# Optimization experiments

Hardware: AMD Instinct MI355X
Metric: run time of the kernel (lower is better)

Reference implementation:

```python
import jax, jax.numpy as jnp
import numpy as np

# Hyperparameters matching init_kwargs
DIM = 1024
HEADS = 16
MEM_HIDDEN = 512
FF_DIM = 4096
CHUNK = 128
NPERSIST = 16
ALPHA = 0.02
THETA = 0.1
ETA = 0.9
B, T = 2, 1024


def _mem_read(x, p):
    """DeepMemory forward: 2-layer MLP dim->hidden->dim with SiLU between."""
    W1, b1, W2, b2 = p
    h = jax.nn.silu(x @ W1.T + b1)
    return h @ W2.T + b2


def setup_inputs() -> dict:
    key = jax.random.key(0)
    ks = jax.random.split(key, 16)
    s = 0.02  # weight init scale
    return {
        "x": jax.random.normal(ks[0], (B, T, DIM), jnp.float32),
        "Wqkv": jax.random.normal(ks[1], (3 * DIM, DIM), jnp.float32) * s,
        "mW1": jax.random.normal(ks[2], (MEM_HIDDEN, DIM), jnp.float32) * s,
        "mb1": jnp.zeros((MEM_HIDDEN,), jnp.float32),
        "mW2": jax.random.normal(ks[3], (DIM, MEM_HIDDEN), jnp.float32) * s,
        "mb2": jnp.zeros((DIM,), jnp.float32),
        "P": jax.random.normal(ks[4], (1, NPERSIST, DIM), jnp.float32),
        "Wqkv_attn": jax.random.normal(ks[5], (3 * DIM, DIM), jnp.float32) * s,
        "Wo": jax.random.normal(ks[6], (DIM, DIM), jnp.float32) * s,
        "ffW1": jax.random.normal(ks[7], (FF_DIM, DIM), jnp.float32) * s,
        "ffb1": jnp.zeros((FF_DIM,), jnp.float32),
        "ffW2": jax.random.normal(ks[8], (DIM, FF_DIM), jnp.float32) * s,
        "ffb2": jnp.zeros((DIM,), jnp.float32),
    }


def reference(x, Wqkv, mW1, mb1, mW2, mb2, P, Wqkv_attn, Wo, ffW1, ffb1, ffW2, ffb2):
    Bb, Tt, D = x.shape
    nC = Tt // CHUNK

    # shared qkv projection (bias-free Linear)
    qkv = x @ Wqkv.T                       # [B,T,3D]
    K = qkv[..., D:2 * D]
    V = qkv[..., 2 * D:]

    # chunked test-time memory writes: k,v are detached in the torch code
    Kc = jax.lax.stop_gradient(K).reshape(Bb, nC, CHUNK, D).transpose(1, 0, 2, 3)  # [nC,B,C,D]
    Vc = jax.lax.stop_gradient(V).reshape(Bb, nC, CHUNK, D).transpose(1, 0, 2, 3)

    params0 = tuple(jax.lax.stop_gradient(p) for p in (mW1, mb1, mW2, mb2))
    mom0 = tuple(jnp.zeros_like(p) for p in params0)

    def loss_fn(p, k, v):
        return jnp.mean((_mem_read(k, p) - v) ** 2)

    def step(carry, kv):
        p, m = carry
        k, v = kv
        g = jax.grad(loss_fn)(p, k, v)
        # momentum: s = eta*s - theta*g ; weight: w = (1-alpha)*w + s
        m = tuple(ETA * mi - THETA * gi for mi, gi in zip(m, g))
        p = tuple((1.0 - ALPHA) * pi + mi for pi, mi in zip(p, m))
        return (p, m), None

    (pf, _), _ = jax.lax.scan(step, (params0, mom0), (Kc, Vc))
    pf = jax.lax.stop_gradient(pf)  # fast weights are buffers (non-differentiable)

    # memory readout tokens for the whole segment
    Q = qkv[..., :D]
    mem_tok = _mem_read(Q, pf)             # [B,T,D]

    # concatenate persistent + memory + input tokens
    tokens = jnp.concatenate([jnp.broadcast_to(P, (Bb, NPERSIST, D)), mem_tok, x], axis=1)
    N = tokens.shape[1]                    # NPERSIST + 2T
    dh = D // HEADS

    # causal multi-head attention over the concatenated sequence
    aqkv = tokens @ Wqkv_attn.T            # [B,N,3D]
    q, k, v = jnp.split(aqkv, 3, axis=-1)
    to_heads = lambda t: t.reshape(Bb, N, HEADS, dh).transpose(0, 2, 1, 3)
    q, k, v = to_heads(q), to_heads(k), to_heads(v)
    scores = jnp.einsum('bhnd,bhmd->bhnm', q, k) / jnp.sqrt(jnp.float32(dh))
    causal = jnp.tril(jnp.ones((N, N), bool))
    scores = jnp.where(causal, scores, jnp.float32(-1e9))
    attn = jax.nn.softmax(scores, axis=-1)
    o = jnp.einsum('bhnm,bhmd->bhnd', attn, v).transpose(0, 2, 1, 3).reshape(Bb, N, D)
    y = o @ Wo.T

    # feed-forward (no residual in source)
    y = jax.nn.gelu(y @ ffW1.T + ffb1) @ ffW2.T + ffb2

    # drop persistent + memory tokens, gate by a fresh memory read
    out = y[:, NPERSIST + Tt:, :]          # [B,T,D]
    newQ = (out @ Wqkv.T)[..., :D]
    return out * _mem_read(newQ, pf)
```

## Files before the change

### kernel.cpp

```cpp
#include <hip/hip_runtime.h>
#include <math.h>

#define BATCH 2
#define TSEQ 1024
#define DIMD 1024
#define NPERS 16
#define NCH 8
#define NTOK 2064
#define ETA_C 0.9f
#define THETA_C 0.1f
#define ALPHA_C 0.02f

typedef __attribute__((ext_vector_type(4))) float f32x4;
typedef __attribute__((ext_vector_type(8))) short s16x8;
typedef unsigned short u16;

__device__ __forceinline__ u16 f2bf(float f) {
    unsigned int u = __float_as_uint(f);
    return (u16)((u + 0x7fffu + ((u >> 16) & 1u)) >> 16);
}
__device__ __forceinline__ float bf2f(u16 h) { return __uint_as_float(((unsigned)h) << 16); }
__device__ __forceinline__ void split2(float v, u16& h, u16& l) {
    h = f2bf(v); l = f2bf(v - bf2f(h));
}

static const size_t oRA = 0;
static const size_t oRB = 50724864;
static const size_t oRC = 67633152;
static const size_t oRD = 80216064;
static const size_t oRE = 96993280;
static const size_t oRF = 109576192;
static const size_t oRG = 113770496;
static const size_t oRH = 117970944;

static const size_t PW1 = 0, PB1 = 524288, PW2 = 524800, PB2 = 1049088, PSZ = 1050112;

__device__ __forceinline__ void gload_lds16(const u16* g, u16* l) {
    __builtin_amdgcn_global_load_lds(
        (const __attribute__((address_space(1))) unsigned int*)g,
        (__attribute__((address_space(3))) unsigned int*)l, 16, 0, 0);
}

__device__ __forceinline__ void xcd_swz2(int cmaj, int& bx, int& by) {
    int gx = gridDim.x, gy = gridDim.y, nwg = gx * gy;
    int lid = cmaj ? (blockIdx.x * gy + blockIdx.y) : (blockIdx.y * gx + blockIdx.x);
    int t = lid;
    if ((nwg & 7) == 0) {
        int q = nwg >> 3;
        t = (lid & 7) * q + (lid >> 3);
    }
    if (cmaj) { by = t % gy; bx = t / gy; }
    else      { bx = t % gx; by = t / gx; }
}
__device__ __forceinline__ void xcd_swizzle(int& bx, int& by) { xcd_swz2(0, bx, by); }

__device__ __forceinline__ void stage_tile(const u16* sp, u16* buf, int rbase,
                                           int M, int clampM, int K, int k0,
                                           int lane) {
    const int lr = lane >> 2, lc = lane & 3;
    #pragma unroll
    for (int i = 0; i < 8; ++i) {
        int r = i * 16 + lr;
        int gr = rbase + r;
        if (clampM && gr >= M) gr = M - 1;
        int g = lc ^ ((r >> 1) & 3);
        gload_lds16(sp + (size_t)gr * K + k0 + g * 8, buf + i * 512);
    }
}

__device__ __forceinline__ void stage_tile64(const u16* sp, u16* buf, int rbase,
                                             int K, int k0, int lane) {
    const int lr = lane >> 3, lc = lane & 7;
    #pragma unroll
    for (int i = 0; i < 16; ++i) {
        int r = i * 8 + lr;
        int gr = rbase + r;
        int g = lc ^ (r & 7);
        gload_lds16(sp + (size_t)gr * K + k0 + g * 8, buf + i * 512);
    }
}

template<int NPROD>
__device__ __forceinline__ void mm_loop32(u16* lds,
                const u16* sp, int rbase, int M, int clampM, int K,
                int kbeg, int kend, int wid, int lane, int wm, int wn,
                f32x4 acc[4][4]) {
    constexpr int TILES = (NPROD == 3) ? 4 : 3;
    constexpr int BUF = TILES * 4096;
    constexpr int WOFF = (NPROD == 3) ? 2 : 1;
    const int frow = lane & 15, kblk = lane >> 4;
    const int nt = (kend - kbeg) >> 5;
    const int doStage = (NPROD == 3) || (wid != 1);
    const int stile = (NPROD == 3) ? wid : ((wid == 0) ? 0 : wid - 1);
    if (doStage) stage_tile(sp, lds + stile * 4096, rbase, M, clampM, K, kbeg, lane);
    for (int t = 0; t < nt; ++t) {
        __syncthreads();
        if (t + 1 < nt && doStage)
            stage_tile(sp, lds + ((t + 1) & 1) * BUF + stile * 4096, rbase, M, clampM, K,
                       kbeg + ((t + 1) << 5), lane);
        const u16* cb = lds + (t & 1) * BUF;
        s16x8 bh[4], bl[4];
        #pragma unroll
        for (int ni = 0; ni < 4; ++ni) {
            int br = wn * 64 + ni * 16 + frow;
            int pc = kblk ^ ((br >> 1) & 3);
            bh[ni] = *(const s16x8*)&cb[WOFF * 4096 + br * 32 + pc * 8];
            bl[ni] = *(const s16x8*)&cb[(WOFF + 1) * 4096 + br * 32 + pc * 8];
        }
        #pragma unroll
        for (int mi = 0; mi < 4; ++mi) {
            int ar = wm * 64 + mi * 16 + frow;
            int pc = kblk ^ ((ar >> 1) & 3);
            s16x8 ah = *(const s16x8*)&cb[0 * 4096 + ar * 32 + pc * 8];
            s16x8 al;
            if (NPROD == 3) al = *(const s16x8*)&cb[1 * 4096 + ar * 32 + pc * 8];
            #pragma unroll
            for (int ni = 0; ni < 4; ++ni) {
                acc[mi][ni] = __builtin_amdgcn_mfma_f32_16x16x32_bf16(ah, bh[ni], acc[mi][ni], 0, 0, 0);
                acc[mi][ni] = __builtin_amdgcn_mfma_f32_16x16x32_bf16(ah, bl[ni], acc[mi][ni], 0, 0, 0);
                if (NPROD == 3)
                    acc[mi][ni] = __builtin_amdgcn_mfma_f32_16x16x32_bf16(al, bh[ni], acc[mi][ni], 0, 0, 0);
            }
        }
    }
}

template<int ACTF, int WF32, int WSPLIT, int PARTIAL, int NPROD>
__global__ __launch_bounds__(256)
void gemm_mfma_k(const u16* __restrict__ Ah, const u16* __restrict__ Al,
                 const u16* __restrict__ Wh, const u16* __restrict__ Wl,
                 float* __restrict__ C, u16* __restrict__ Chi, u16* __restrict__ Clo,
                 int M, int N, int K, const float* __restrict__ bias, int cmaj)
{
    constexpr int TILES = (NPROD == 3) ? 4 : 3;
    __shared__ u16 lds[2 * TILES * 4096];
    const int tid = threadIdx.x;
    const int lane = tid & 63, wid = tid >> 6;
    const int wm = wid >> 1, wn = wid & 1;
    int bx, by; xcd_swz2(cmaj, bx, by);
    const int row0 = by * 128, col0 = bx * 128;
    const u16* sp = (wid == 0) ? Ah : (wid == 1) ? Al : (wid == 2) ? Wh : Wl;
    const int rbase = (wid < 2) ? row0 : col0;
    const int clampM = (wid < 2) ? 1 : 0;
    f32x4 acc[4][4] = {};
    int kbeg = 0, kend = K;
    if (PARTIAL) {
        int Kseg = K / gridDim.z;
        kbeg = blockIdx.z * Kseg;
        kend = kbeg + Kseg;
    }
    mm_loop32<NPROD>(&lds[0], sp, rbase, M, clampM, K, kbeg, kend, wid, lane, wm, wn, acc);

    const int erow = (lane >> 4) * 4, ecol = lane & 15;
    #pragma unroll
    for (int mi = 0; mi < 4; ++mi) {
        #pragma unroll
        for (int ni = 0; ni < 4; ++ni) {
            int c = col0 + wn * 64 + ni * 16 + ecol;
            float bv = (!PARTIAL && bias) ? bias[c] : 0.f;
            #pragma unroll
            for (int reg = 0; reg < 4; ++reg) {
                int r = row0 + wm * 64 + mi * 16 + erow + reg;
                if (r >= M) continue;
                float v = acc[mi][ni][reg] + bv;
                if (PARTIAL) {
                    C[((size_t)blockIdx.z * M + r) * N + c] = v;
                    continue;
                }
                if (ACTF == 1) v = v / (1.f + __expf(-v));
                else if (ACTF == 2) {
                    float u = 0.7978845608028654f * (v + 0.044715f * v * v * v);
                    v = 0.5f * v * (1.f + tanhf(u));
                }
                size_t o = (size_t)r * N + c;
                if (WF32) C[o] = v;
                if (WSPLIT) { u16 h, l; split2(v, h, l); Chi[o] = h; Clo[o] = l; }
            }
        }
    }
}

__global__ __launch_bounds__(256)
void gemm_qkv_k(const u16* __restrict__ Ah, const u16* __restrict__ Al,
                const u16* __restrict__ Wh, const u16* __restrict__ Wl,
                u16* __restrict__ Qh, u16* __restrict__ Ql,
                u16* __restrict__ kch, u16* __restrict__ kcl,
                u16* __restrict__ kcTh, u16* __restrict__ kcTl,
                float* __restrict__ Vb, int M, int N, int K)
{
    __shared__ u16 lds[2 * 3 * 4096];
    const int tid = threadIdx.x;
    const int lane = tid & 63, wid = tid >> 6;
    const int wm = wid >> 1, wn = wid & 1;
    int bx, by; xcd_swz2(1, bx, by);
    const int row0 = by * 128, col0 = bx * 128;
    const u16* sp = (wid == 0) ? Ah : (wid == 1) ? Al : (wid == 2) ? Wh : Wl;
    const int rbase = (wid < 2) ? row0 : col0;
    f32x4 acc[4][4] = {};
    mm_loop32<2>(&lds[0], sp, rbase, M, 0, K, 0, K, wid, lane, wm, wn, acc);

    const int erow = (lane >> 4) * 4, ecol = lane & 15;
    #pragma unroll
    for (int mi = 0; mi < 4; ++mi) {
        #pragma unroll
        for (int ni = 0; ni < 4; ++ni) {
            int c = col0 + wn * 64 + ni * 16 + ecol;
            #pragma unroll
            for (int reg = 0; reg < 4; ++reg) {
                int r = row0 + wm * 64 + mi * 16 + erow + reg;
                float v = acc[mi][ni][reg];
                int b = r >> 10, t = r & 1023;
                if (c < 1024) {
                    size_t o = (size_t)r * 1024 + c;
                    Qh[o] = f2bf(v);
                } else if (c < 2048) {
                    int d = c - 1024;
                    int ch = t >> 7, rr = t & 127;
                    size_t o = ((size_t)((ch * 2 + b) * 128 + rr)) * 1024 + d;
                    u16 h, l; split2(v, h, l);
                    kch[o] = h;
                    size_t ot = (size_t)ch * 262144 + (size_t)d * 256 + b * 128 + rr;
                    kcTh[ot] = h; kcTl[ot] = l;
                } else {
                    int d = c - 2048;
                    int ch = t >> 7, rr = t & 127;
                    Vb[((size_t)((ch * 2 + b) * 128 + rr)) * 1024 + d] = v;
                }
            }
        }
    }
}

__global__ __launch_bounds__(256)
void gemm_aqkv_k(const u16* __restrict__ Ah, const u16* __restrict__ Al,
                 const u16* __restrict__ Wh, const u16* __restrict__ Wl,
                 u16* __restrict__ fQh, u16* __restrict__ fQl,
                 u16* __restrict__ fKh, u16* __restrict__ fKl,
                 u16* __restrict__ fVt, int M, int N, int K)
{
    __shared__ u16 lds[2 * 3 * 4096];
    const int tid = threadIdx.x;
    const int lane = tid & 63, wid = tid >> 6;
    const int wm = wid >> 1, wn = wid & 1;
    int bx, by; xcd_swz2(1, bx, by);
    if (bx < 8 && ((by <= 7) || (by >= 17 && by <= 23))) return;
    const int row0 = by * 128, col0 = bx * 128;
    const u16* sp = (wid == 0) ? Ah : (wid == 1) ? Al : (wid == 2) ? Wh : Wl;
    const int rbase = (wid < 2) ? row0 : col0;
    const int clampM = (wid < 2) ? 1 : 0;
    f32x4 acc[4][4] = {};
    mm_loop32<2>(&lds[0], sp, rbase, M, clampM, K, 0, K, wid, lane, wm, wn, acc);

    const int erow = (lane >> 4) * 4, ecol = lane & 15;
    #pragma unroll
    for (int mi = 0; mi < 4; ++mi) {
        #pragma unroll
        for (int ni = 0; ni < 4; ++ni) {
            int c = col0 + wn * 64 + ni * 16 + ecol;
            #pragma unroll
            for (int reg = 0; reg < 4; ++reg) {
                int r = row0 + wm * 64 + mi * 16 + erow + reg;
                if (r >= M) continue;
                float v = acc[mi][ni][reg];
                int b = (r >= 2064) ? 1 : 0;
                int n = r - b * 2064;
                if (c < 1024) {
                    if (n >= NPERS + TSEQ) {
                        int h = c >> 6, d = c & 63;
                        int row = n - (NPERS + TSEQ);
                        size_t o = (((size_t)(b * 16 + h)) * 1024 + row) * 64 + d;
                        u16 hh, ll; split2(0.125f * v, hh, ll);
                        fQh[o] = hh; fQl[o] = ll;
                    }
                } else if (c < 2048) {
                    int cc = c - 1024;
                    int h = cc >> 6, d = cc & 63;
                    size_t o = (((size_t)(b * 16 + h)) * NTOK + n) * 64 + d;
                    u16 hh, ll; split2(v, hh, ll);
                    fKh[o] = hh; fKl[o] = ll;
                } else {
                    int cc = c - 2048;
                    int h = cc >> 6, d = cc & 63;
                    fVt[(((size_t)(b * 16 + h)) * 64 + d) * NTOK + n] = f2bf(v);
                }
            }
        }
    }
}

template<int ACTF, int WF32, int WSPLIT>
__global__ __launch_bounds__(256)
void reduce_k(const float* __restrict__ Cp, int S,
              float* __restrict__ C, u16* __restrict__ Chi, u16* __restrict__ Clo,
              const float* __restrict__ bias, int M, int N)
{
    int i = blockIdx.x * 256 + threadIdx.x;
    int n4 = (int)((size_t)M * N / 4);
    if (i >= n4) return;
    size_t off = (size_t)i * 4;
    float4 v = *(const float4*)&Cp[off];
    for (int z = 1; z < S; ++z) {
        float4 u = *(const float4*)&Cp[(size_t)z * M * N + off];
        v.x += u.x; v.y += u.y; v.z += u.z; v.w += u.w;
    }
    int c = (int)(off % N);
    float vv[4] = {v.x, v.y, v.z, v.w};
    #pragma unroll
    for (int j = 0; j < 4; ++j) {
        float w = vv[j];
        if (bias) w += bias[c + j];
        if (ACTF == 1) w = w / (1.f + __expf(-w));
        else if (ACTF == 2) {
            float u = 0.7978845608028654f * (w + 0.044715f * w * w * w);
            w = 0.5f * w * (1.f + tanhf(u));
        }
        if (WF32) C[off + j] = w;
        if (WSPLIT) { u16 h, l; split2(w, h, l); Chi[off + j] = h; Clo[off + j] = l; }
    }
}

__global__ __launch_bounds__(256)
void reduce_tok_k(const float* __restrict__ Cp, const float* __restrict__ bias,
                  u16* __restrict__ th, u16* __restrict__ tl)
{
    int i = blockIdx.x * 256 + threadIdx.x;
    if (i >= 524288) return;
    size_t off = (size_t)i * 4;
    float4 v = *(const float4*)&Cp[off];
    float4 u = *(const float4*)&Cp[2097152 + off];
    v.x += u.x; v.y += u.y; v.z += u.z; v.w += u.w;
    int r = (int)(off >> 10), c = (int)(off & 1023);
    int b = r >> 10, t = r & 1023;
    size_t orow = (((size_t)(b * NTOK + NPERS + t)) << 10) + c;
    float vv[4] = {v.x + bias[c], v.y + bias[c + 1], v.z + bias[c + 2], v.w + bias[c + 3]};
    u16 h0,l0,h1,l1,h2,l2,h3,l3;
    split2(vv[0],h0,l0); split2(vv[1],h1,l1); split2(vv[2],h2,l2); split2(vv[3],h3,l3);
    ushort4 hv = {h0,h1,h2,h3}, lv = {l0,l1,l2,l3};
    *(ushort4*)&th[orow] = hv;
    *(ushort4*)&tl[orow] = lv;
}

static void gemm_mfma(hipStream_t s, int act, int wf32, int wsplit,
                      const u16* Ah, const u16* Al, const u16* Wh, const u16* Wl,
                      float* C, u16* Ch, u16* Cl, int M, int N, int K,
                      const float* bias, int nprod = 3, int cmaj = 0)
{
    dim3 g(N / 128, (M + 127) / 128), b(256);
    if (act == 0 && wf32 == 1 && wsplit == 0)
        gemm_mfma_k<0,1,0,0,3><<<g,b,0,s>>>(Ah,Al,Wh,Wl,C,Ch,Cl,M,N,K,bias,cmaj);
    else if (act == 0 && wf32 == 1 && wsplit == 1)
        gemm_mfma_k<0,1,1,0,3><<<g,b,0,s>>>(Ah,Al,Wh,Wl,C,Ch,Cl,M,N,K,bias,cmaj);
    else if (act == 0 && wf32 == 0 && wsplit == 1)
        gemm_mfma_k<0,0,1,0,3><<<g,b,0,s>>>(Ah,Al,Wh,Wl,C,Ch,Cl,M,N,K,bias,cmaj);
    else if (act == 1)
        gemm_mfma_k<1,0,1,0,3><<<g,b,0,s>>>(Ah,Al,Wh,Wl,C,Ch,Cl,M,N,K,bias,cmaj);
    else if (nprod == 2)
        gemm_mfma_k<2,0,1,0,2><<<g,b,0,s>>>(Ah,Al,Wh,Wl,C,Ch,Cl,M,N,K,bias,cmaj);
    else
        gemm_mfma_k<2,0,1,0,3><<<g,b,0,s>>>(Ah,Al,Wh,Wl,C,Ch,Cl,M,N,K,bias,cmaj);
}

static void gemm_mfma_sk(hipStream_t s, int act, int wf32, int wsplit,
                         const u16* Ah, const u16* Al, const u16* Wh, const u16* Wl,
                         float* C, u16* Ch, u16* Cl, int M, int N, int K,
                         const float* bias, int S, float* part, int nprod = 3,
                         int cmaj = 0)
{
    if (S <= 1) { gemm_mfma(s, act, wf32, wsplit, Ah, Al, Wh, Wl, C, Ch, Cl, M, N, K, bias, nprod, cmaj); return; }
    dim3 g(N / 128, (M + 127) / 128, S), b(256);
    if (nprod == 2)
        gemm_mfma_k<0,0,0,1,2><<<g,b,0,s>>>(Ah,Al,Wh,Wl,part,nullptr,nullptr,M,N,K,nullptr,cmaj);
    else
        gemm_mfma_k<0,0,0,1,3><<<g,b,0,s>>>(Ah,Al,Wh,Wl,part,nullptr,nullptr,M,N,K,nullptr,cmaj);
    int n4 = (int)((size_t)M * N / 4);
    dim3 rg((n4 + 255) / 256), rb(256);
    if (act == 0 && wf32 == 1 && wsplit == 0)
        reduce_k<0,1,0><<<rg,rb,0,s>>>(part, S, C, Ch, Cl, bias, M, N);
    else if (act == 0 && wf32 == 1 && wsplit == 1)
        reduce_k<0,1,1><<<rg,rb,0,s>>>(part, S, C, Ch, Cl, bias, M, N);
    else if (act == 0 && wf32 == 0 && wsplit == 1)
        reduce_k<0,0,1><<<rg,rb,0,s>>>(part, S, C, Ch, Cl, bias, M, N);
    else if (act == 1)
        reduce_k<1,0,1><<<rg,rb,0,s>>>(part, S, C, Ch, Cl, bias, M, N);
    else
        reduce_k<2,0,1><<<rg,rb,0,s>>>(part, S, C, Ch, Cl, bias, M, N);
}

template<int MODE, int NPROD>
__device__ __forceinline__ void scan_body(u16* lds, int bx, int by,
                 const u16* __restrict__ Ah, const u16* __restrict__ Al,
                 const u16* __restrict__ Wh, const u16* __restrict__ Wl,
                 float* __restrict__ C, u16* __restrict__ Chi, u16* __restrict__ Clo,
                 u16* __restrict__ ChiT, u16* __restrict__ CloT,
                 const float* __restrict__ Zf, const float* __restrict__ add,
                 const float* __restrict__ bias, float* __restrict__ CP,
                 int M, int N, int K, float alpha)
{
    constexpr int TILES = (NPROD == 3) ? 4 : 3;
    constexpr int BUF = TILES * 8192;
    constexpr int WOFF = (NPROD == 3) ? 2 : 1;
    const int tid = threadIdx.x;
    const int lane = tid & 63, wid = tid >> 6;
    const int wm = wid >> 1, wn = wid & 1;
    const int row0 = by * 128, col0 = bx * 128;

    const u16* sp = (wid == 0) ? Ah : (wid == 1) ? Al : (wid == 2) ? Wh : Wl;
    const int rbase = (wid < 2) ? row0 : col0;
    const int doStage = (NPROD == 3) || (wid != 1);
    const int stile = (NPROD == 3) ? wid : ((wid == 0) ? 0 : wid - 1);

    f32x4 acc[4][4] = {};
    const int frow = lane & 15, kblk = lane >> 4;
    const int nt = K >> 6;

    if (doStage) stage_tile64(sp, lds + stile * 8192, rbase, K, 0, lane);

    for (int t = 0; t < nt; ++t) {
        __syncthreads();
        if (t + 1 < nt && doStage)
            stage_tile64(sp, lds + ((t + 1) & 1) * BUF + stile * 8192, rbase, K,
                         (t + 1) << 6, lane);
        const u16* cb = lds + (t & 1) * BUF;

        #pragma unroll
        for (int s = 0; s < 2; ++s) {
            s16x8 bh[4], bl[4];
            #pragma unroll
            for (int ni = 0; ni < 4; ++ni) {
                int br = wn * 64 + ni * 16 + frow;
                int pc = (s * 4 + kblk) ^ (br & 7);
                bh[ni] = *(const s16x8*)&cb[WOFF * 8192 + br * 64 + pc * 8];
                bl[ni] = *(const s16x8*)&cb[(WOFF + 1) * 8192 + br * 64 + pc * 8];
            }
            #pragma unroll
            for (int mi = 0; mi < 4; ++mi) {
                int ar = wm * 64 + mi * 16 + frow;
                int pc = (s * 4 + kblk) ^ (ar & 7);
                s16x8 ah = *(const s16x8*)&cb[0 * 8192 + ar * 64 + pc * 8];
                s16x8 al;
                if (NPROD == 3) al = *(const s16x8*)&cb[1 * 8192 + ar * 64 + pc * 8];
                #pragma unroll
                for (int ni = 0; ni < 4; ++ni) {
                    acc[mi][ni] = __builtin_amdgcn_mfma_f32_16x16x32_bf16(ah, bh[ni], acc[mi][ni], 0, 0, 0);
                    acc[mi][ni] = __builtin_amdgcn_mfma_f32_16x16x32_bf16(ah, bl[ni], acc[mi][ni], 0, 0, 0);
                    if (NPROD == 3)
                        acc[mi][ni] = __builtin_amdgcn_mfma_f32_16x16x32_bf16(al, bh[ni], acc[mi][ni], 0, 0, 0);
                }
            }
        }
    }

    const int erow = (lane >> 4) * 4, ecol = lane & 15;
    float csum[4] = {0.f, 0.f, 0.f, 0.f};
    #pragma unroll
    for (int mi = 0; mi < 4; ++mi) {
        #pragma unroll
        for (int ni = 0; ni < 4; ++ni) {
            int c = col0 + wn * 64 + ni * 16 + ecol;
            #pragma unroll
            for (int reg = 0; reg < 4; ++reg) {
                int r = row0 + wm * 64 + mi * 16 + erow + reg;
                float v = acc[mi][ni][reg];
                size_t o = (size_t)r * N + c;
                if (MODE == 1) {
                    v += bias[c];
                    C[o] = v;
                    float hv = v / (1.f + __expf(-v));
                    u16 h, l; split2(hv, h, l);
                    Chi[o] = h; Clo[o] = l;
                    size_t ot = (size_t)c * M + r;
                    ChiT[ot] = h; CloT[ot] = l;
                } else if (MODE == 2) {
                    v += bias[c] - add[o];
                    u16 h, l; split2(v, h, l);
                    Chi[o] = h; Clo[o] = l;
                    size_t ot = (size_t)c * M + r;
                    ChiT[ot] = h; CloT[ot] = l;
                    csum[ni] += v;
                } else if (MODE == 3) {
                    C[o] = alpha * v;
                } else {
                    v *= alpha;
                    float z = Zf[o];
                    float sg = 1.f / (1.f + __expf(-z));
                    v *= sg * (1.f + z * (1.f - sg));
                    u16 h, l; split2(v, h, l);
                    size_t ot = (size_t)c * M + r;
                    ChiT[ot] = h; CloT[ot] = l;
                    csum[ni] += v;
                }
            }
        }
    }
    if (MODE == 2 || MODE == 4) {
        #pragma unroll
        for (int ni = 0; ni < 4; ++ni) {
            float s = csum[ni];
            s += __shfl_xor(s, 16);
            s += __shfl_xor(s, 32);
            if ((lane >> 4) == 0) {
                int c = col0 + wn * 64 + ni * 16 + ecol;
                float w = (MODE == 2) ? alpha * s : s;
                CP[(size_t)(by * 2 + wm) * N + c] = w;
            }
        }
    }
}

template<int MODE>
__global__ __launch_bounds__(256)
void gemm_scan_k(const u16* __restrict__ Ah, const u16* __restrict__ Al,
                 const u16* __restrict__ Wh, const u16* __restrict__ Wl,
                 float* __restrict__ C, u16* __restrict__ Chi, u16* __restrict__ Clo,
                 u16* __restrict__ ChiT, u16* __restrict__ CloT,
                 const float* __restrict__ Zf, const float* __restrict__ add,
                 const float* __restrict__ bias, float* __restrict__ CP,
                 int M, int N, int K, float alpha)
{
    __shared__ u16 lds[2 * 3 * 8192];
    int bx, by; xcd_swizzle(bx, by);
    scan_body<MODE, 2>(&lds[0], bx, by, Ah, Al, Wh, Wl, C, Chi, Clo, ChiT, CloT,
                       Zf, add, bias, CP, M, N, K, alpha);
}

__global__ __launch_bounds__(256)
void gemm_scan_pair_k(const u16* __restrict__ rTh, const u16* __restrict__ rTl,
                      const u16* __restrict__ hTh, const u16* __restrict__ hTl,
                      float* __restrict__ gW2,
                      const u16* __restrict__ rh_, const u16* __restrict__ rl_,
                      const u16* __restrict__ w2th, const u16* __restrict__ w2tl,
                      u16* __restrict__ dhTh, u16* __restrict__ dhTl,
                      const float* __restrict__ z1, float* __restrict__ cp1, float cs)
{
    __shared__ u16 lds[2 * 3 * 8192];
    if (blockIdx.y < 8) {
        scan_body<3, 2>(&lds[0], blockIdx.x, blockIdx.y, rTh, rTl, hTh, hTl,
                        gW2, nullptr, nullptr, nullptr, nullptr, nullptr, nullptr,
                        nullptr, nullptr, 1024, 512, 256, cs);
    } else {
        scan_body<4, 2>(&lds[0], blockIdx.x, blockIdx.y - 8, rh_, rl_, w2th, w2tl,
                        nullptr, nullptr, nullptr, dhTh, dhTl, z1, nullptr,
                        nullptr, cp1, 256, 512, 1024, cs);
    }
}

__global__ void cvt_split_k(const float* __restrict__ in, u16* __restrict__ hi,
                            u16* __restrict__ lo, int n4) {
    int i = blockIdx.x * 256 + threadIdx.x;
    if (i >= n4) return;
    float4 v = *(const float4*)&in[(size_t)i * 4];
    u16 h0,l0,h1,l1,h2,l2,h3,l3;
    split2(v.x,h0,l0); split2(v.y,h1,l1); split2(v.z,h2,l2); split2(v.w,h3,l3);
    ushort4 hv = {h0,h1,h2,h3}, lv = {l0,l1,l2,l3};
    *(ushort4*)&hi[(size_t)i * 4] = hv;
    *(ushort4*)&lo[(size_t)i * 4] = lv;
}
__global__ void transpose_split_k(const float* __restrict__ in, u16* __restrict__ outh,
                                  u16* __restrict__ outl, int R, int C) {
    __shared__ float t[32][33];
    const int c0 = blockIdx.x * 32, r0 = blockIdx.y * 32;
    const size_t zoff = (size_t)blockIdx.z * R * C;
    const int tx = threadIdx.x & 31, ty = threadIdx.x >> 5;
    #pragma unroll
    for (int p = 0; p < 4; ++p) {
        int r = ty + p * 8;
        t[r][tx] = in[zoff + (size_t)(r0 + r) * C + c0 + tx];
    }
    __syncthreads();
    #pragma unroll
    for (int p = 0; p < 4; ++p) {
        int cc = ty + p * 8;
        float v = t[tx][cc];
        u16 h, l; split2(v, h, l);
        size_t o = zoff + (size_t)(c0 + cc) * R + r0 + tx;
        outh[o] = h; outl[o] = l;
    }
}
__global__ void update3_k(float* __restrict__ p, float* __restrict__ mo,
                          const float* __restrict__ g,
                          const float* __restrict__ cp1, const float* __restrict__ cp2,
                          u16* __restrict__ w1h, u16* __restrict__ w1l,
                          u16* __restrict__ w2h, u16* __restrict__ w2l,
                          u16* __restrict__ w2th, u16* __restrict__ w2tl, int n) {
    int i = blockIdx.x * 256 + threadIdx.x;
    if (i >= n) return;
    float gi;
    if (i < 524288) gi = g[i];
    else if (i < 524800) {
        int j = i - 524288;
        gi = cp1[j] + cp1[512 + j] + cp1[1024 + j] + cp1[1536 + j];
    } else if (i < 1049088) gi = g[i];
    else {
        int j = i - 1049088;
        gi = cp2[j] + cp2[1024 + j] + cp2[2048 + j] + cp2[3072 + j];
    }
    float m = ETA_C * mo[i] - THETA_C * gi;
    mo[i] = m;
    float pv = (1.f - ALPHA_C) * p[i] + m;
    p[i] = pv;
    if (i < 524288) {
        u16 h, l; split2(pv, h, l); w1h[i] = h; w1l[i] = l;
    } else if (i >= 524800 && i < 1049088) {
        int j = i - 524800;
        u16 h, l; split2(pv, h, l);
        w2h[j] = h; w2l[j] = l;
        int tj = (j & 511) * 1024 + (j >> 9);
        w2th[tj] = h; w2tl[tj] = l;
    }
}
__global__ void tokens_px_k(const float* __restrict__ P, const float* __restrict__ x,
                            u16* __restrict__ th, u16* __restrict__ tl) {
    size_t idx = (size_t)blockIdx.x * 256 + threadIdx.x;
    if (idx >= (size_t)2 * 1040 * 1024) return;
    int d = (int)(idx & 1023);
    int rl = (int)((idx >> 10) % 1040);
    int b = (int)(idx / ((size_t)1040 * 1024));
    float v; int n;
    if (rl < NPERS) { v = P[(size_t)rl * 1024 + d]; n = rl; }
    else { int t = rl - NPERS; v = x[((size_t)b * TSEQ + t) * 1024 + d]; n = NPERS + TSEQ + t; }
    size_t o = (((size_t)(b * NTOK + n)) << 10) + d;
    u16 h, l; split2(v, h, l); th[o] = h; tl[o] = l;
}
__global__ void mul_k(const float* __restrict__ a, const float* __restrict__ b,
                      float* __restrict__ o, int n) {
    int i = blockIdx.x * 256 + threadIdx.x;
    if (i < n) o[i] = a[i] * b[i];
}

__global__ __launch_bounds__(256)
void flash_part_k(const u16* __restrict__ Qsh, const u16* __restrict__ Qsl,
                  const u16* __restrict__ Ksh, const u16* __restrict__ Ksl,
                  const u16* __restrict__ Vts, float* __restrict__ Of,
                  float* __restrict__ Lf)
{
    __shared__ u16 lds[16384];
    u16* KH = lds;            u16* KL = lds + 4096;
    u16* VT = lds + 8192;
    u16* PH = lds + 12288;

    int lid = blockIdx.x + (blockIdx.y << 4) + (blockIdx.z << 8);
    int t1024 = ((lid & 7) << 7) | (lid >> 3);
    const int qt = t1024 & 15, h = (t1024 >> 4) & 15;
    const int zb = t1024 >> 8;
    const int b = zb >> 1, z = zb & 1;

    const int tid = threadIdx.x;
    const int lane = tid & 63, wid = tid >> 6;
    const int fr = lane & 15, kq = lane >> 4;
    const int bh = b * 16 + h;
    const int q0c = qt * 64;
    const int q0a = NPERS + TSEQ + q0c;
    const int ntile = ((q0a + 63) >> 6) + 1;
    const int half = ntile >> 1;
    const int jt0 = z ? half : 0;
    const int jt1 = z ? ntile : half;
    const int l8 = lane & 7, lr8 = lane >> 3;

    auto stageKV = [&](int jt) {
        const int j0 = jt * 64;
        #pragma unroll
        for (int jj = 0; jj < 6; ++jj) {
            int j = wid * 6 + jj;
            int buf = j >> 3, i8 = j & 7;
            if (buf < 2) {
                int row = i8 * 8 + lr8;
                int grow = j0 + row; if (grow > NTOK - 1) grow = NTOK - 1;
                int c = l8 ^ (row & 7);
                const u16* src = (buf == 0 ? Ksh : Ksl) +
                                 (((size_t)bh * NTOK + grow) << 6) + c * 8;
                gload_lds16(src, (buf == 0 ? KH : KL) + i8 * 512);
            } else {
                int d = i8 * 8 + lr8;
                int c = l8 ^ (d & 7);
                int col = j0 + c * 8; if (col > NTOK - 8) col = NTOK - 8;
                const u16* src = Vts + ((size_t)bh * 64 + d) * NTOK + col;
                gload_lds16(src, VT + i8 * 512);
            }
        }
    };

    s16x8 qh[2], ql[2];
    {
        const size_t qrow = ((size_t)bh * 1024 + q0c + wid * 16 + fr) << 6;
        #pragma unroll
        for (int kb = 0; kb < 2; ++kb) {
            qh[kb] = *(const s16x8*)&Qsh[qrow + (size_t)(kb * 4 + kq) * 8];
            ql[kb] = *(const s16x8*)&Qsl[qrow + (size_t)(kb * 4 + kq) * 8];
        }
    }

    s16x8 ones;
    #pragma unroll
    for (int i = 0; i < 8; ++i) ones[i] = (short)0x3F80;

    f32x4 Oa[4] = {};
    f32x4 lacc = {};

    for (int jt = jt0; jt < jt1; ++jt) {
        const int j0 = jt * 64;
        stageKV(jt);
        __syncthreads();

        f32x4 sacc[4] = {};
        __builtin_amdgcn_s_setprio(1);
        #pragma unroll
        for (int nt = 0; nt < 4; ++nt) {
            #pragma unroll
            for (int kb = 0; kb < 2; ++kb) {
                int br = nt * 16 + fr;
                int sl = (kb * 4 + kq) ^ (fr & 7);
                s16x8 kh = *(const s16x8*)&KH[br * 64 + sl * 8];
                s16x8 kl = *(const s16x8*)&KL[br * 64 + sl * 8];
                sacc[nt] = __builtin_amdgcn_mfma_f32_16x16x32_bf16(qh[kb], kh, sacc[nt], 0, 0, 0);
                sacc[nt] = __builtin_amdgcn_mfma_f32_16x16x32_bf16(ql[kb], kh, sacc[nt], 0, 0, 0);
                sacc[nt] = __builtin_amdgcn_mfma_f32_16x16x32_bf16(qh[kb], kl, sacc[nt], 0, 0, 0);
            }
        }
        __builtin_amdgcn_s_setprio(0);

        #pragma unroll
        for (int r = 0; r < 4; ++r) {
            const int qloc = kq * 4 + r;
            const int qi = q0a + wid * 16 + qloc;
            const int prow = wid * 16 + qloc;
            #pragma unroll
            for (int nt = 0; nt < 4; ++nt) {
                int kj = j0 + nt * 16 + fr;
                float e = (kj <= qi) ? __expf(sacc[nt][r]) : 0.f;
                int col = nt * 16 + fr;
                int sl = (col >> 3) ^ (qloc & 7);
                PH[prow * 64 + sl * 8 + (col & 7)] = f2bf(e);
            }
        }

        __builtin_amdgcn_s_setprio(1);
        #pragma unroll
        for (int kb = 0; kb < 2; ++kb) {
            int pr = wid * 16 + fr;
            int sl = (kb * 4 + kq) ^ (fr & 7);
            s16x8 pa = *(const s16x8*)&PH[pr * 64 + sl * 8];
            lacc = __builtin_amdgcn_mfma_f32_16x16x32_bf16(pa, ones, lacc, 0, 0, 0);
            #pragma unroll
            for (int dt = 0; dt < 4; ++dt) {
                int vr = dt * 16 + fr;
                s16x8 vb = *(const s16x8*)&VT[vr * 64 + sl * 8];
                Oa[dt] = __builtin_amdgcn_mfma_f32_16x16x32_bf16(pa, vb, Oa[dt], 0, 0, 0);
            }
        }
        __builtin_amdgcn_s_setprio(0);
        __syncthreads();
    }

    const size_t obase = ((((size_t)z * 2 + b) * 16 + h) * 16 + qt) * 4096;
    const size_t mlb   = ((((size_t)z * 2 + b) * 16 + h) * 16 + qt) * 64;
    #pragma unroll
    for (int r = 0; r < 4; ++r) {
        int rl = wid * 16 + kq * 4 + r;
        if (fr == 0) Lf[mlb + rl] = lacc[r];
        #pragma unroll
        for (int dt = 0; dt < 4; ++dt)
            Of[obase + (size_t)rl * 64 + dt * 16 + fr] = Oa[dt][r];
    }
}

__global__ __launch_bounds__(256)
void flash_merge_k(const float* __restrict__ Of, const float* __restrict__ Lf,
                   u16* __restrict__ oh, u16* __restrict__ ol)
{
    const int qt = blockIdx.x, h = blockIdx.y, b = blockIdx.z;
    const int tid = threadIdx.x;
    const int row = tid >> 2, quad = tid & 3;
    const size_t b0 = ((((size_t)0 * 2 + b) * 16 + h) * 16 + qt) * 4096 + (size_t)row * 64;
    const size_t b1 = ((((size_t)1 * 2 + b) * 16 + h) * 16 + qt) * 4096 + (size_t)row * 64;
    const size_t m0i = ((((size_t)0 * 2 + b) * 16 + h) * 16 + qt) * 64 + row;
    const size_t m1i = ((((size_t)1 * 2 + b) * 16 + h) * 16 + qt) * 64 + row;
    float inv = 1.f / (Lf[m0i] + Lf[m1i]);
    const size_t orow = ((size_t)(b * 1024 + qt * 64 + row)) * 1024 + h * 64;
    #pragma unroll
    for (int i = 0; i < 4; ++i) {
        int col = quad * 16 + i * 4;
        float4 v0 = *(const float4*)&Of[b0 + col];
        float4 v1 = *(const float4*)&Of[b1 + col];
        float o0 = (v0.x + v1.x) * inv;
        float o1 = (v0.y + v1.y) * inv;
        float o2 = (v0.z + v1.z) * inv;
        float o3 = (v0.w + v1.w) * inv;
        u16 h0,l0_,h1,l1_,h2,l2_,h3,l3_;
        split2(o0,h0,l0_); split2(o1,h1,l1_); split2(o2,h2,l2_); split2(o3,h3,l3_);
        ushort4 hv = {h0,h1,h2,h3}, lv = {l0_,l1_,l2_,l3_};
        *(ushort4*)&oh[orow + col] = hv;
        *(ushort4*)&ol[orow + col] = lv;
    }
}

extern "C" void kernel_launch(void* const* d_in, const int* in_sizes, int n_in,
                              void* d_out, int out_size, void* d_ws, size_t ws_size,
                              hipStream_t stream)
{
    const float* x     = (const float*)d_in[0];
    const float* Wqkv  = (const float*)d_in[1];
    const float* mW1   = (const float*)d_in[2];
    const float* mb1   = (const float*)d_in[3];
    const float* mW2   = (const float*)d_in[4];
    const float* mb2   = (const float*)d_in[5];
    const float* Pp    = (const float*)d_in[6];
    const float* Wqa   = (const float*)d_in[7];
    const float* Wo    = (const float*)d_in[8];
    const float* ffW1  = (const float*)d_in[9];
    const float* ffb1  = (const float*)d_in[10];
    const float* ffW2  = (const float*)d_in[11];
    const float* ffb2  = (const float*)d_in[12];
    char* wsb = (char*)d_ws;
    float* outp = (float*)d_out;

    float* z1    = (float*)(wsb + oRA);
    float* grd   = (float*)(wsb + oRA + 3145728);
    float* cp2   = (float*)(wsb + oRA + 7346176);
    float* cp1   = (float*)(wsb + oRA + 7362560);
    u16* hh_     = (u16*)(wsb + oRA + 8388608);
    u16* hl_     = (u16*)(wsb + oRA + 8650752);
    u16* hTh     = (u16*)(wsb + oRA + 9437184);
    u16* hTl     = (u16*)(wsb + oRA + 9699328);
    u16* rh_     = (u16*)(wsb + oRA + 10485760);
    u16* rl_     = (u16*)(wsb + oRA + 11010048);
    u16* rTh     = (u16*)(wsb + oRA + 11534336);
    u16* rTl     = (u16*)(wsb + oRA + 12058624);
    u16* dhTh    = (u16*)(wsb + oRA + 12582912);
    u16* dhTl    = (u16*)(wsb + oRA + 12845056);
    u16* kcTh    = (u16*)(wsb + oRA + 16777216);
    u16* kcTl    = (u16*)(wsb + oRA + 20971520);
    float* Of    = (float*)(wsb + oRA);
    float* Lf    = (float*)(wsb + oRA + 16777216);
    u16* fVth    = (u16*)(wsb + oRA + 17825792);
    u16* fKl     = (u16*)(wsb + oRA + 26279936);
    u16* Woh     = (u16*)(wsb + oRA);
    u16* Wol     = (u16*)(wsb + oRA + 2097152);
    u16* ffhh    = (u16*)(wsb + oRA);
    u16* ffhl    = (u16*)(wsb + oRA + 16777216);
    u16* outbh   = (u16*)(wsb + oRA + 33554432);
    u16* outbl   = (u16*)(wsb + oRA + 37748736);
    u16* newQh   = (u16*)(wsb + oRA);
    u16* newQl   = (u16*)(wsb + oRA + 4194304);
    u16* hzh     = (u16*)(wsb + oRA + 8388608);
    u16* hzl     = (u16*)(wsb + oRA + 10485760);
    float* memq  = (float*)(wsb + oRA + 12582912);
    float* partA0 = (float*)(wsb + oRA);
    float* partA1 = (float*)(wsb + oRA + 4194304);
    float* partA2 = (float*)(wsb + oRA + 16777216);
    float* Vb    = (float*)(wsb + oRB + 8388608);
    u16* tokh    = (u16*)(wsb + oRB);
    u16* tokl    = (u16*)(wsb + oRB + 8454144);
    u16* oh      = (u16*)(wsb + oRB);
    u16* ol      = (u16*)(wsb + oRB + 4194304);
    u16* y1h     = (u16*)(wsb + oRB + 8388608);
    u16* y1l     = (u16*)(wsb + oRB + 12582912);
    float* partB = (float*)(wsb + oRB);
    u16* xh      = (u16*)(wsb + oRC);
    u16* xl      = (u16*)(wsb + oRC + 4194304);
    float* mom   = (float*)(wsb + oRC);
    u16* pW2Th   = (u16*)(wsb + oRC + 5242880);
    u16* pW2Tl   = (u16*)(wsb + oRC + 6291456);
    u16* Wqah    = (u16*)(wsb + oRC);
    u16* Wqal    = (u16*)(wsb + oRC + 6291456);
    u16* Qh      = (u16*)(wsb + oRD);
    u16* Ql      = (u16*)(wsb + oRD + 4194304);
    u16* kchh    = (u16*)(wsb + oRD + 8388608);
    u16* kchl    = (u16*)(wsb + oRD + 12582912);
    u16* t1h     = (u16*)(wsb + oRD + 8388608);
    u16* t1l     = (u16*)(wsb + oRD + 10485760);
    u16* fKh     = (u16*)(wsb + oRD);
    u16* ffW1h   = (u16*)(wsb + oRD);
    u16* ffW1l   = (u16*)(wsb + oRD + 8388608);
    u16* ffW2h   = (u16*)(wsb + oRD);
    u16* ffW2l   = (u16*)(wsb + oRD + 8388608);
    u16* Wqkvh   = (u16*)(wsb + oRE);
    u16* Wqkvl   = (u16*)(wsb + oRE + 6291456);
    u16* pW1h    = (u16*)(wsb + oRF);
    u16* pW1l    = (u16*)(wsb + oRF + 1048576);
    u16* pW2h    = (u16*)(wsb + oRF + 2097152);
    u16* pW2l    = (u16*)(wsb + oRF + 3145728);
    float* par   = (float*)(wsb + oRG);
    float* outb  = (float*)(wsb + oRH);
    u16* fQh     = (u16*)(wsb + oRH);
    u16* fQl     = (u16*)(wsb + oRH + 4194304);

    hipMemcpyAsync(par + PW1, mW1, 524288 * sizeof(float), hipMemcpyDeviceToDevice, stream);
    hipMemcpyAsync(par + PB1, mb1, 512 * sizeof(float), hipMemcpyDeviceToDevice, stream);
    hipMemcpyAsync(par + PW2, mW2, 524288 * sizeof(float), hipMemcpyDeviceToDevice, stream);
    hipMemcpyAsync(par + PB2, mb2, 1024 * sizeof(float), hipMemcpyDeviceToDevice, stream);

    cvt_split_k<<<2048, 256, 0, stream>>>(x, xh, xl, 524288);
    cvt_split_k<<<3072, 256, 0, stream>>>(Wqkv, Wqkvh, Wqkvl, 786432);
    gemm_qkv_k<<<dim3(24, 16), 256, 0, stream>>>(xh, xl, Wqkvh, Wqkvl,
        Qh, Ql, kchh, kchl, kcTh, kcTl, Vb, 2048, 3072, 1024);

    hipMemsetAsync(mom, 0, PSZ * sizeof(float), stream);
    cvt_split_k<<<512, 256, 0, stream>>>(par + PW1, pW1h, pW1l, 131072);
    cvt_split_k<<<512, 256, 0, stream>>>(par + PW2, pW2h, pW2l, 131072);
    transpose_split_k<<<dim3(16, 32, 1), 256, 0, stream>>>(par + PW2, pW2Th, pW2Tl, 1024, 512);

    const float cs = 2.f / (float)(BATCH * 128 * DIMD);
    for (int c = 0; c < NCH; ++c) {
        const u16* kch = kchh + (size_t)c * 262144;
        const u16* kcl = kchl + (size_t)c * 262144;
        const u16* kth = kcTh + (size_t)c * 262144;
        const u16* ktl = kcTl + (size_t)c * 262144;
        const float* vc = Vb + (size_t)c * 262144;
        gemm_scan_k<1><<<dim3(4, 2), 256, 0, stream>>>(kch, kcl, pW1h, pW1l,
            z1, hh_, hl_, hTh, hTl, nullptr, nullptr, par + PB1, nullptr, 256, 512, 1024, 1.f);
        gemm_scan_k<2><<<dim3(8, 2), 256, 0, stream>>>(hh_, hl_, pW2h, pW2l,
            nullptr, rh_, rl_, rTh, rTl, nullptr, vc, par + PB2, cp2, 256, 1024, 512, cs);
        gemm_scan_pair_k<<<dim3(4, 10), 256, 0, stream>>>(rTh, rTl, hTh, hTl, grd + PW2,
            rh_, rl_, pW2Th, pW2Tl, dhTh, dhTl, z1, cp1, cs);
        gemm_scan_k<3><<<dim3(8, 4), 256, 0, stream>>>(dhTh, dhTl, kth, ktl,
            grd + PW1, nullptr, nullptr, nullptr, nullptr, nullptr, nullptr, nullptr, nullptr,
            512, 1024, 256, 1.f);
        update3_k<<<4102, 256, 0, stream>>>(par, mom, grd, cp1, cp2,
            pW1h, pW1l, pW2h, pW2l, pW2Th, pW2Tl, (int)PSZ);
    }

    gemm_mfma_sk(stream, 1, 0, 1, Qh, Ql, pW1h, pW1l, nullptr, t1h, t1l,
                 2048, 512, 1024, par + PB1, 4, partA2, 2);
    {
        dim3 g(8, 16, 2), b(256);
        gemm_mfma_k<0,0,0,1,2><<<g, b, 0, stream>>>(t1h, t1l, pW2h, pW2l,
            partA0, nullptr, nullptr, 2048, 1024, 512, nullptr, 0);
        reduce_tok_k<<<2048, 256, 0, stream>>>(partA0, par + PB2, tokh, tokl);
    }

    tokens_px_k<<<8320, 256, 0, stream>>>(Pp, x, tokh, tokl);
    cvt_split_k<<<3072, 256, 0, stream>>>(Wqa, Wqah, Wqal, 786432);
    gemm_aqkv_k<<<dim3(24, 33), 256, 0, stream>>>(tokh, tokl, Wqah, Wqal,
        fQh, fQl, fKh, fKl, fVth, 4128, 3072, 1024);

    flash_part_k<<<dim3(16, 16, 4), 256, 0, stream>>>(fQh, fQl, fKh, fKl, fVth, Of, Lf);
    flash_merge_k<<<dim3(16, 16, 2), 256, 0, stream>>>(Of, Lf, oh, ol);

    cvt_split_k<<<1024, 256, 0, stream>>>(Wo, Woh, Wol, 262144);
    gemm_mfma_sk(stream, 0, 0, 1, oh, ol, Woh, Wol, nullptr, y1h, y1l,
                 2048, 1024, 1024, nullptr, 2, partA1, 2);
    cvt_split_k<<<4096, 256, 0, stream>>>(ffW1, ffW1h, ffW1l, 1048576);
    gemm_mfma(stream, 2, 0, 1, y1h, y1l, ffW1h, ffW1l, nullptr, ffhh, ffhl,
              2048, 4096, 1024, ffb1, 2, 1);
    cvt_split_k<<<4096, 256, 0, stream>>>(ffW2, ffW2h, ffW2l, 1048576);
    gemm_mfma_sk(stream, 0, 1, 1, ffhh, ffhl, ffW2h, ffW2l, outb, outbh, outbl,
                 2048, 1024, 4096, ffb2, 2, partB, 2);

    gemm_mfma_sk(stream, 0, 0, 1, outbh, outbl, Wqkvh, Wqkvl, nullptr, newQh, newQl,
                 2048, 1024, 1024, nullptr, 2, partB, 2);
    gemm_mfma_sk(stream, 1, 0, 1, newQh, newQl, pW1h, pW1l, nullptr, hzh, hzl,
                 2048, 512, 1024, par + PB1, 4, partB, 2);
    gemm_mfma_sk(stream, 0, 1, 0, hzh, hzl, pW2h, pW2l, memq, nullptr, nullptr,
                 2048, 1024, 512, par + PB2, 2, partB, 3);
    mul_k<<<8192, 256, 0, stream>>>(outb, memq, outp, 2097152);
}
```

Before: 1.153 ms.

## Fuse gW1 GEMM with momentum update and drop Q low-part in attention

Each memory chunk's gW1 GEMM epilogue now applies the momentum and weight update directly, and extra blocks in the same launch update W2 and the biases. This replaces a separate GEMM plus an elementwise update kernel and removes the gW1 gradient round-trip through global memory and one launch per chunk. Separately, the attention Q operand is stored only as a single bf16 value, dropping one of three split-precision MFMAs in the score computation. That lowers Q·K accuracy relative to the previous three-product emulation.

```diff
diff --git a/kernel.cpp b/kernel.cpp
--- a/kernel.cpp
+++ b/kernel.cpp
@@ -269,8 +269,7 @@
                         int h = c >> 6, d = c & 63;
                         int row = n - (NPERS + TSEQ);
                         size_t o = (((size_t)(b * 16 + h)) * 1024 + row) * 64 + d;
-                        u16 hh, ll; split2(0.125f * v, hh, ll);
-                        fQh[o] = hh; fQl[o] = ll;
+                        fQh[o] = f2bf(0.125f * v);
                     }
                 } else if (c < 2048) {
                     int cc = c - 1024;
@@ -394,6 +393,7 @@
                  u16* __restrict__ ChiT, u16* __restrict__ CloT,
                  const float* __restrict__ Zf, const float* __restrict__ add,
                  const float* __restrict__ bias, float* __restrict__ CP,
+                 float* __restrict__ MO,
                  int M, int N, int K, float alpha)
 {
     constexpr int TILES = (NPROD == 3) ? 4 : 3;
@@ -479,6 +479,13 @@
                     csum[ni] += v;
                 } else if (MODE == 3) {
                     C[o] = alpha * v;
+                } else if (MODE == 6) {
+                    float m = ETA_C * MO[o] - THETA_C * v;
+                    MO[o] = m;
+                    float pv = (1.f - ALPHA_C) * C[o] + m;
+                    C[o] = pv;
+                    u16 h, l; split2(pv, h, l);
+                    Chi[o] = h; Clo[o] = l;
                 } else {
                     v *= alpha;
                     float z = Zf[o];
@@ -520,7 +527,7 @@
     __shared__ u16 lds[2 * 3 * 8192];
     int bx, by; xcd_swizzle(bx, by);
     scan_body<MODE, 2>(&lds[0], bx, by, Ah, Al, Wh, Wl, C, Chi, Clo, ChiT, CloT,
-                       Zf, add, bias, CP, M, N, K, alpha);
+                       Zf, add, bias, CP, nullptr, M, N, K, alpha);
 }
 
 __global__ __launch_bounds__(256)
@@ -536,11 +543,62 @@
     if (blockIdx.y < 8) {
         scan_body<3, 2>(&lds[0], blockIdx.x, blockIdx.y, rTh, rTl, hTh, hTl,
                         gW2, nullptr, nullptr, nullptr, nullptr, nullptr, nullptr,
-                        nullptr, nullptr, 1024, 512, 256, cs);
+                        nullptr, nullptr, nullptr, 1024, 512, 256, cs);
     } else {
         scan_body<4, 2>(&lds[0], blockIdx.x, blockIdx.y - 8, rh_, rl_, w2th, w2tl,
                         nullptr, nullptr, nullptr, dhTh, dhTl, z1, nullptr,
-                        nullptr, cp1, 256, 512, 1024, cs);
+                        nullptr, cp1, nullptr, 256, 512, 1024, cs);
+    }
+}
+
+__global__ __launch_bounds__(256)
+void gemm_gw1up_k(const u16* __restrict__ dhTh, const u16* __restrict__ dhTl,
+                  const u16* __restrict__ kth, const u16* __restrict__ ktl,
+                  float* __restrict__ par, float* __restrict__ mo,
+                  u16* __restrict__ w1h, u16* __restrict__ w1l,
+                  u16* __restrict__ w2h, u16* __restrict__ w2l,
+                  u16* __restrict__ w2th, u16* __restrict__ w2tl,
+                  const float* __restrict__ g2,
+                  const float* __restrict__ cp1, const float* __restrict__ cp2)
+{
+    __shared__ u16 lds[2 * 3 * 8192];
+    const int tid = threadIdx.x;
+    if (blockIdx.y < 4) {
+        scan_body<6, 2>(&lds[0], blockIdx.x, blockIdx.y, dhTh, dhTl, kth, ktl,
+                        par, w1h, w1l, nullptr, nullptr, nullptr, nullptr,
+                        nullptr, nullptr, mo, 512, 1024, 256, 1.f);
+    } else {
+        int uid = (blockIdx.y - 4) * 8 + blockIdx.x;
+        #pragma unroll
+        for (int it = 0; it < 32; ++it) {
+            int j = uid * 8192 + it * 256 + tid;
+            float gi = g2[j];
+            size_t i = 524800 + (size_t)j;
+            float m = ETA_C * mo[i] - THETA_C * gi;
+            mo[i] = m;
+            float pv = (1.f - ALPHA_C) * par[i] + m;
+            par[i] = pv;
+            u16 h, l; split2(pv, h, l);
+            w2h[j] = h; w2l[j] = l;
+            int tj = (j & 511) * 1024 + (j >> 9);
+            w2th[tj] = h; w2tl[tj] = l;
+        }
+        if (uid == 0) {
+            for (int jj = tid; jj < 1536; jj += 256) {
+                size_t i; float gi;
+                if (jj < 512) {
+                    i = 524288 + jj;
+                    gi = cp1[jj] + cp1[512 + jj] + cp1[1024 + jj] + cp1[1536 + jj];
+                } else {
+                    int j2 = jj - 512;
+                    i = 1049088 + j2;
+                    gi = cp2[j2] + cp2[1024 + j2] + cp2[2048 + j2] + cp2[3072 + j2];
+                }
+                float m = ETA_C * mo[i] - THETA_C * gi;
+                mo[i] = m;
+                par[i] = (1.f - ALPHA_C) * par[i] + m;
+            }
+        }
     }
 }
 
@@ -574,38 +632,6 @@
         u16 h, l; split2(v, h, l);
         size_t o = zoff + (size_t)(c0 + cc) * R + r0 + tx;
         outh[o] = h; outl[o] = l;
-    }
-}
-__global__ void update3_k(float* __restrict__ p, float* __restrict__ mo,
-                          const float* __restrict__ g,
-                          const float* __restrict__ cp1, const float* __restrict__ cp2,
-                          u16* __restrict__ w1h, u16* __restrict__ w1l,
-                          u16* __restrict__ w2h, u16* __restrict__ w2l,
-                          u16* __restrict__ w2th, u16* __restrict__ w2tl, int n) {
-    int i = blockIdx.x * 256 + threadIdx.x;
-    if (i >= n) return;
-    float gi;
-    if (i < 524288) gi = g[i];
-    else if (i < 524800) {
-        int j = i - 524288;
-        gi = cp1[j] + cp1[512 + j] + cp1[1024 + j] + cp1[1536 + j];
-    } else if (i < 1049088) gi = g[i];
-    else {
-        int j = i - 1049088;
-        gi = cp2[j] + cp2[1024 + j] + cp2[2048 + j] + cp2[3072 + j];
-    }
-    float m = ETA_C * mo[i] - THETA_C * gi;
-    mo[i] = m;
-    float pv = (1.f - ALPHA_C) * p[i] + m;
-    p[i] = pv;
-    if (i < 524288) {
-        u16 h, l; split2(pv, h, l); w1h[i] = h; w1l[i] = l;
-    } else if (i >= 524800 && i < 1049088) {
-        int j = i - 524800;
-        u16 h, l; split2(pv, h, l);
-        w2h[j] = h; w2l[j] = l;
-        int tj = (j & 511) * 1024 + (j >> 9);
-        w2th[tj] = h; w2tl[tj] = l;
     }
 }
 __global__ void tokens_px_k(const float* __restrict__ P, const float* __restrict__ x,
@@ -628,7 +654,7 @@
 }
 
 __global__ __launch_bounds__(256)
-void flash_part_k(const u16* __restrict__ Qsh, const u16* __restrict__ Qsl,
+void flash_part_k(const u16* __restrict__ Qsh,
                   const u16* __restrict__ Ksh, const u16* __restrict__ Ksl,
                   const u16* __restrict__ Vts, float* __restrict__ Of,
                   float* __restrict__ Lf)
@@ -679,14 +705,12 @@
         }
     };
 
-    s16x8 qh[2], ql[2];
+    s16x8 qh[2];
     {
         const size_t qrow = ((size_t)bh * 1024 + q0c + wid * 16 + fr) << 6;
         #pragma unroll
-        for (int kb = 0; kb < 2; ++kb) {
+        for (int kb = 0; kb < 2; ++kb)
             qh[kb] = *(const s16x8*)&Qsh[qrow + (size_t)(kb * 4 + kq) * 8];
-            ql[kb] = *(const s16x8*)&Qsl[qrow + (size_t)(kb * 4 + kq) * 8];
-        }
     }
 
     s16x8 ones;
@@ -712,7 +736,6 @@
                 s16x8 kh = *(const s16x8*)&KH[br * 64 + sl * 8];
                 s16x8 kl = *(const s16x8*)&KL[br * 64 + sl * 8];
                 sacc[nt] = __builtin_amdgcn_mfma_f32_16x16x32_bf16(qh[kb], kh, sacc[nt], 0, 0, 0);
-                sacc[nt] = __builtin_amdgcn_mfma_f32_16x16x32_bf16(ql[kb], kh, sacc[nt], 0, 0, 0);
                 sacc[nt] = __builtin_amdgcn_mfma_f32_16x16x32_bf16(qh[kb], kl, sacc[nt], 0, 0, 0);
             }
         }
@@ -912,11 +935,8 @@
             nullptr, rh_, rl_, rTh, rTl, nullptr, vc, par + PB2, cp2, 256, 1024, 512, cs);
         gemm_scan_pair_k<<<dim3(4, 10), 256, 0, stream>>>(rTh, rTl, hTh, hTl, grd + PW2,
             rh_, rl_, pW2Th, pW2Tl, dhTh, dhTl, z1, cp1, cs);
-        gemm_scan_k<3><<<dim3(8, 4), 256, 0, stream>>>(dhTh, dhTl, kth, ktl,
-            grd + PW1, nullptr, nullptr, nullptr, nullptr, nullptr, nullptr, nullptr, nullptr,
-            512, 1024, 256, 1.f);
-        update3_k<<<4102, 256, 0, stream>>>(par, mom, grd, cp1, cp2,
-            pW1h, pW1l, pW2h, pW2l, pW2Th, pW2Tl, (int)PSZ);
+        gemm_gw1up_k<<<dim3(8, 12), 256, 0, stream>>>(dhTh, dhTl, kth, ktl,
+            par, mom, pW1h, pW1l, pW2h, pW2l, pW2Th, pW2Tl, grd + PW2, cp1, cp2);
     }
 
     gemm_mfma_sk(stream, 1, 0, 1, Qh, Ql, pW1h, pW1l, nullptr, t1h, t1l,
@@ -933,7 +953,7 @@
     gemm_aqkv_k<<<dim3(24, 33), 256, 0, stream>>>(tokh, tokl, Wqah, Wqal,
         fQh, fQl, fKh, fKl, fVth, 4128, 3072, 1024);
 
-    flash_part_k<<<dim3(16, 16, 4), 256, 0, stream>>>(fQh, fQl, fKh, fKl, fVth, Of, Lf);
+    flash_part_k<<<dim3(16, 16, 4), 256, 0, stream>>>(fQh, fKh, fKl, fVth, Of, Lf);
     flash_merge_k<<<dim3(16, 16, 2), 256, 0, stream>>>(Of, Lf, oh, ol);
 
     cvt_split_k<<<1024, 256, 0, stream>>>(Wo, Woh, Wol, 262144);
```

After: 1.202 ms. 4.3% more time.
